# Optimization experiments

Hardware: AMD Instinct MI355X
Metric: run time of the kernel (lower is better)

The kernel has to match this reference:

```python
import jax, jax.numpy as jnp
import numpy as np

N = 100000
E = 800000
NODE_DIM = 128
EDGE_DIM = 8
NUM_HEADS = 8
HEAD_DIM = NODE_DIM // NUM_HEADS


def setup_inputs() -> dict:
    key = jax.random.key(0)
    k_x, k_ei, k_ea, k_w1, k_b1, k_w2, k_b2 = jax.random.split(key, 7)
    x = jax.random.normal(k_x, (N, NODE_DIM), dtype=jnp.float32)
    edge_index = jax.random.randint(k_ei, (2, E), 0, N, dtype=jnp.int32)
    edge_attr = jax.random.normal(k_ea, (E, EDGE_DIM), dtype=jnp.float32)
    # node_proj: Linear(node_dim, node_dim)
    lim1 = 1.0 / np.sqrt(NODE_DIM)
    W_node = jax.random.uniform(k_w1, (NODE_DIM, NODE_DIM), minval=-lim1, maxval=lim1, dtype=jnp.float32)
    b_node = jax.random.uniform(k_b1, (NODE_DIM,), minval=-lim1, maxval=lim1, dtype=jnp.float32)
    # edge_to_attn: Linear(edge_dim, num_heads) followed by sigmoid
    lim2 = 1.0 / np.sqrt(EDGE_DIM)
    W_edge = jax.random.uniform(k_w2, (NUM_HEADS, EDGE_DIM), minval=-lim2, maxval=lim2, dtype=jnp.float32)
    b_edge = jax.random.uniform(k_b2, (NUM_HEADS,), minval=-lim2, maxval=lim2, dtype=jnp.float32)
    return {"x": x, "edge_index": edge_index, "edge_attr": edge_attr,
            "W_node": W_node, "b_node": b_node, "W_edge": W_edge, "b_edge": b_edge}


def reference(x, edge_index, edge_attr, W_node, b_node, W_edge, b_edge):
    # project node features: [N, node_dim]
    x_proj = x @ W_node.T + b_node
    # per-edge, per-head sigmoid gates: [E, H]
    edge_gates = jax.nn.sigmoid(edge_attr @ W_edge.T + b_edge)
    source = edge_index[0]
    target = edge_index[1]
    # gather source node features: [E, H, head_dim]
    x_source = x_proj[source].reshape(E, NUM_HEADS, HEAD_DIM)
    # gate and flatten messages: [E, node_dim]
    messages = (x_source * edge_gates[:, :, None]).reshape(E, NODE_DIM)
    # scatter-add to target nodes: [N, node_dim]
    out = jax.ops.segment_sum(messages, target, num_segments=N)
    return out
```

## Files before the change

### kernel.cpp

```cpp
#include <hip/hip_runtime.h>

typedef unsigned char u8;
typedef unsigned short u16;
typedef unsigned int u32;
typedef __attribute__((ext_vector_type(8))) short short8;
typedef __attribute__((ext_vector_type(4))) float f32x4;

constexpr int NODES = 100000;
constexpr int EDGES = 800000;
constexpr int DIM = 128;
constexpr int EDIM = 8;
constexpr int HEADS = 8;

constexpr int PROJ_BLOCKS = (NODES + 127) / 128;
constexpr int REC_BLOCKS  = (EDGES + 255) / 256;

__device__ inline u16 f2bf(float f) {
    u32 u = __float_as_uint(f);
    u = (u + 0x7FFFu + ((u >> 16) & 1u)) >> 16;
    return (u16)u;
}
__device__ inline float bf2f(u16 s) {
    return __uint_as_float(((u32)s) << 16);
}

__global__ __launch_bounds__(256) void prep_fused(const float* __restrict__ x,
                                                  const float* __restrict__ Wn,
                                                  const float* __restrict__ bn,
                                                  const int* __restrict__ ei,
                                                  const float* __restrict__ ea,
                                                  const float* __restrict__ We,
                                                  const float* __restrict__ be,
                                                  int* __restrict__ head4,
                                                  uint4* __restrict__ recE,
                                                  u16* __restrict__ xpb) {
    __shared__ u16 sLds[64 * 136];

    const int tid = threadIdx.x;

    if (blockIdx.x < PROJ_BLOCKS) {
        if (blockIdx.x == 0 && tid == 0) {
            recE[-1] = uint4{(u32)-1, 0u, 0u, 0u};
        }

        const int w = tid >> 6;
        const int l = tid & 63;
        const int lr = l & 15;
        const int lh = l >> 4;
        const int m0 = blockIdx.x * 128 + w * 32;

        f32x4 acc[2][8];
        #pragma unroll
        for (int mt = 0; mt < 2; ++mt)
            #pragma unroll
            for (int nt = 0; nt < 8; ++nt) acc[mt][nt] = f32x4{0, 0, 0, 0};

        #pragma unroll
        for (int half = 0; half < 2; ++half) {
            __syncthreads();
            {
                #pragma unroll
                for (int i = tid; i < 64 * 16; i += 256) {
                    int row = i >> 4, ch = i & 15;
                    const float* p = Wn + (half * 64 + row) * DIM + ch * 8;
                    float4 f0 = *reinterpret_cast<const float4*>(p);
                    float4 f1 = *reinterpret_cast<const float4*>(p + 4);
                    short8 v;
                    v[0]=(short)f2bf(f0.x); v[1]=(short)f2bf(f0.y);
                    v[2]=(short)f2bf(f0.z); v[3]=(short)f2bf(f0.w);
                    v[4]=(short)f2bf(f1.x); v[5]=(short)f2bf(f1.y);
                    v[6]=(short)f2bf(f1.z); v[7]=(short)f2bf(f1.w);
                    *reinterpret_cast<short8*>(&sLds[row * 136 + ch * 8]) = v;
                }
            }
            __syncthreads();

            #pragma unroll
            for (int kk = 0; kk < 4; ++kk) {
                const int kb = kk * 32 + lh * 8;
                short8 a0, a1;
                {
                    int row = m0 + lr;  row = row < NODES ? row : 0;
                    const float* p = x + (size_t)row * DIM + kb;
                    float4 f0 = *reinterpret_cast<const float4*>(p);
                    float4 f1 = *reinterpret_cast<const float4*>(p + 4);
                    a0[0]=(short)f2bf(f0.x); a0[1]=(short)f2bf(f0.y);
                    a0[2]=(short)f2bf(f0.z); a0[3]=(short)f2bf(f0.w);
                    a0[4]=(short)f2bf(f1.x); a0[5]=(short)f2bf(f1.y);
                    a0[6]=(short)f2bf(f1.z); a0[7]=(short)f2bf(f1.w);
                }
                {
                    int row = m0 + 16 + lr;  row = row < NODES ? row : 0;
                    const float* p = x + (size_t)row * DIM + kb;
                    float4 f0 = *reinterpret_cast<const float4*>(p);
                    float4 f1 = *reinterpret_cast<const float4*>(p + 4);
                    a1[0]=(short)f2bf(f0.x); a1[1]=(short)f2bf(f0.y);
                    a1[2]=(short)f2bf(f0.z); a1[3]=(short)f2bf(f0.w);
                    a1[4]=(short)f2bf(f1.x); a1[5]=(short)f2bf(f1.y);
                    a1[6]=(short)f2bf(f1.z); a1[7]=(short)f2bf(f1.w);
                }
                #pragma unroll
                for (int nt = 0; nt < 4; ++nt) {
                    const int ntg = half * 4 + nt;
                    short8 b = *reinterpret_cast<const short8*>(
                        &sLds[(nt * 16 + lr) * 136 + kb]);
                    acc[0][ntg] = __builtin_amdgcn_mfma_f32_16x16x32_bf16(a0, b, acc[0][ntg], 0, 0, 0);
                    acc[1][ntg] = __builtin_amdgcn_mfma_f32_16x16x32_bf16(a1, b, acc[1][ntg], 0, 0, 0);
                }
            }
        }

        float bias[8];
        #pragma unroll
        for (int nt = 0; nt < 8; ++nt) bias[nt] = bn[nt * 16 + lr];

        #pragma unroll
        for (int mt = 0; mt < 2; ++mt) {
            #pragma unroll
            for (int r = 0; r < 4; ++r) {
                int grow = m0 + mt * 16 + lh * 4 + r;
                if (grow < NODES) {
                    #pragma unroll
                    for (int nt = 0; nt < 8; ++nt)
                        xpb[(size_t)grow * DIM + nt * 16 + lr] =
                            f2bf(acc[mt][nt][r] + bias[nt]);
                }
            }
        }
    } else {
        float* sW = reinterpret_cast<float*>(sLds);
        float* sb = sW + HEADS * EDIM;
        if (tid < HEADS * EDIM) sW[tid] = We[tid];
        if (tid < HEADS) sb[tid] = be[tid];
        __syncthreads();

        const int e = (blockIdx.x - PROJ_BLOCKS) * 256 + tid;
        if (e >= EDGES) return;

        const int src = ei[e];
        const int tgt = ei[EDGES + e];
        float4 a0 = *reinterpret_cast<const float4*>(ea + (size_t)e * EDIM);
        float4 a1 = *reinterpret_cast<const float4*>(ea + (size_t)e * EDIM + 4);

        u32 q[HEADS];
        #pragma unroll
        for (int h = 0; h < HEADS; ++h) {
            const float* w = &sW[h * EDIM];
            float z = sb[h]
                    + a0.x * w[0] + a0.y * w[1] + a0.z * w[2] + a0.w * w[3]
                    + a1.x * w[4] + a1.y * w[5] + a1.z * w[6] + a1.w * w[7];
            float g = 1.0f / (1.0f + __expf(-z));
            q[h] = (u32)(g * 255.0f + 0.5f);
        }

        int nx = atomicExch(&head4[tgt * 4 + (e & 3)], e);

        uint4 r;
        r.x = (u32)nx;
        r.y = (u32)(src * DIM);
        r.z = q[0] | (q[1] << 8) | (q[2] << 16) | (q[3] << 24);
        r.w = q[4] | (q[5] << 8) | (q[6] << 16) | (q[7] << 24);
        recE[e] = r;
    }
}

__global__ __launch_bounds__(256) void aggregate_v10(const u16* __restrict__ xpb,
                                                     const int* __restrict__ head4,
                                                     const uint4* __restrict__ recE,
                                                     float* __restrict__ out) {
    const int n = blockIdx.x * 16 + (threadIdx.x >> 4);
    if (n >= NODES) return;
    const int l = threadIdx.x & 15;
    const int h = l >> 1;
    const int hsh = (h & 3) * 8;
    const bool hlo = (h < 4);

    float acc[8];
    #pragma unroll
    for (int i = 0; i < 8; ++i) acc[i] = 0.0f;

    int e0 = head4[n * 4 + 0];
    int e1 = head4[n * 4 + 1];
    int e2 = head4[n * 4 + 2];
    int e3 = head4[n * 4 + 3];

    while ((e0 & e1 & e2 & e3) != -1) {
        uint4 R0 = recE[(ptrdiff_t)e0];
        uint4 R1 = recE[(ptrdiff_t)e1];
        uint4 R2 = recE[(ptrdiff_t)e2];
        uint4 R3 = recE[(ptrdiff_t)e3];
        float g0 = (float)(((hlo ? R0.z : R0.w) >> hsh) & 0xFF);
        float g1 = (float)(((hlo ? R1.z : R1.w) >> hsh) & 0xFF);
        float g2 = (float)(((hlo ? R2.z : R2.w) >> hsh) & 0xFF);
        float g3 = (float)(((hlo ? R3.z : R3.w) >> hsh) & 0xFF);
        short8 u0 = *reinterpret_cast<const short8*>(xpb + R0.y + l * 8);
        short8 u1 = *reinterpret_cast<const short8*>(xpb + R1.y + l * 8);
        short8 u2 = *reinterpret_cast<const short8*>(xpb + R2.y + l * 8);
        short8 u3 = *reinterpret_cast<const short8*>(xpb + R3.y + l * 8);
        #pragma unroll
        for (int i = 0; i < 8; ++i) {
            acc[i] += g0 * bf2f((u16)u0[i]);
            acc[i] += g1 * bf2f((u16)u1[i]);
            acc[i] += g2 * bf2f((u16)u2[i]);
            acc[i] += g3 * bf2f((u16)u3[i]);
        }
        e0 = (int)R0.x;
        e1 = (int)R1.x;
        e2 = (int)R2.x;
        e3 = (int)R3.x;
    }

    constexpr float DQ = 1.0f / 255.0f;
    float4 o0 = {acc[0] * DQ, acc[1] * DQ, acc[2] * DQ, acc[3] * DQ};
    float4 o1 = {acc[4] * DQ, acc[5] * DQ, acc[6] * DQ, acc[7] * DQ};
    float4* op = reinterpret_cast<float4*>(out + (size_t)n * DIM + l * 8);
    op[0] = o0;
    op[1] = o1;
}

__global__ __launch_bounds__(256) void edge_scatter(const int* __restrict__ ei,
                                                    const float* __restrict__ ea,
                                                    const float* __restrict__ We,
                                                    const float* __restrict__ be,
                                                    const u16* __restrict__ xpb,
                                                    float* __restrict__ out) {
    __shared__ float sW[HEADS * EDIM];
    __shared__ float sb[HEADS];
    if (threadIdx.x < HEADS * EDIM) sW[threadIdx.x] = We[threadIdx.x];
    if (threadIdx.x < HEADS) sb[threadIdx.x] = be[threadIdx.x];
    __syncthreads();

    const int t = blockIdx.x * 256 + threadIdx.x;
    const int e = t >> 5;
    const int l = t & 31;
    if (e >= EDGES) return;

    const int src = ei[e];
    const int tgt = ei[EDGES + e];
    const int h = l >> 2;

    float4 ea0 = *reinterpret_cast<const float4*>(ea + (size_t)e * EDIM);
    float4 ea1 = *reinterpret_cast<const float4*>(ea + (size_t)e * EDIM + 4);
    float4 wa = *reinterpret_cast<const float4*>(&sW[h * EDIM]);
    float4 wb = *reinterpret_cast<const float4*>(&sW[h * EDIM + 4]);
    float z = sb[h]
            + ea0.x * wa.x + ea0.y * wa.y + ea0.z * wa.z + ea0.w * wa.w
            + ea1.x * wb.x + ea1.y * wb.y + ea1.z * wb.z + ea1.w * wb.w;
    float g = 1.0f / (1.0f + __expf(-z));

    ushort4 u = *reinterpret_cast<const ushort4*>(xpb + (size_t)src * DIM + l * 4);
    float* op = out + (size_t)tgt * DIM + l * 4;
    unsafeAtomicAdd(op + 0, bf2f(u.x) * g);
    unsafeAtomicAdd(op + 1, bf2f(u.y) * g);
    unsafeAtomicAdd(op + 2, bf2f(u.z) * g);
    unsafeAtomicAdd(op + 3, bf2f(u.w) * g);
}

extern "C" void kernel_launch(void* const* d_in, const int* in_sizes, int n_in,
                              void* d_out, int out_size, void* d_ws, size_t ws_size,
                              hipStream_t stream) {
    const float* x   = (const float*)d_in[0];
    const int*   ei  = (const int*)d_in[1];
    const float* eat = (const float*)d_in[2];
    const float* Wn  = (const float*)d_in[3];
    const float* bn  = (const float*)d_in[4];
    const float* We  = (const float*)d_in[5];
    const float* be  = (const float*)d_in[6];
    float* out = (float*)d_out;

    u16* xpb   = (u16*)d_ws;
    int* head4 = (int*)(xpb + (size_t)NODES * DIM);
    char* recS = (char*)(head4 + (size_t)NODES * 4);
    uint4* recE = (uint4*)(recS + 16);

    const size_t need = (size_t)NODES * DIM * 2 + (size_t)NODES * 16
                      + (size_t)(EDGES + 1) * 16;
    const size_t need_fb = (size_t)NODES * DIM * 2;

    if (ws_size >= need) {
        hipMemsetAsync(head4, 0xFF, (size_t)NODES * 16, stream);
        prep_fused<<<PROJ_BLOCKS + REC_BLOCKS, 256, 0, stream>>>(
            x, Wn, bn, ei, eat, We, be, head4, recE, xpb);
        aggregate_v10<<<(NODES + 15) / 16, 256, 0, stream>>>(xpb, head4, recE, out);
    } else if (ws_size >= need_fb) {
        prep_fused<<<PROJ_BLOCKS, 256, 0, stream>>>(
            x, Wn, bn, ei, eat, We, be, nullptr, recE, xpb);
        hipMemsetAsync(d_out, 0, (size_t)out_size * sizeof(float), stream);
        edge_scatter<<<(EDGES * 32) / 256, 256, 0, stream>>>(ei, eat, We, be, xpb, out);
    }
}
```

Before: 112.7 us.

## Split fused prep kernel, fold head init into projection, stage stores via LDS

Splits the fused projection/edge-record kernel into a dedicated MFMA projection kernel and a separate edge-record kernel. The projection kernel now initializes the head4 list heads itself, replacing the memset launch, and loads the whole bf16 weight matrix into LDS once instead of in two halves. Output tiles are staged through LDS so each row is written with 16-byte global stores rather than scattered 2-byte ones. In exchange it adds a kernel boundary where projection and edge work could previously overlap, and uses more LDS per block, which may lower occupancy.

```diff
diff --git a/kernel.cpp b/kernel.cpp
--- a/kernel.cpp
+++ b/kernel.cpp
@@ -12,9 +12,6 @@
 constexpr int EDIM = 8;
 constexpr int HEADS = 8;
 
-constexpr int PROJ_BLOCKS = (NODES + 127) / 128;
-constexpr int REC_BLOCKS  = (EDGES + 255) / 256;
-
 __device__ inline u16 f2bf(float f) {
     u32 u = __float_as_uint(f);
     u = (u + 0x7FFFu + ((u >> 16) & 1u)) >> 16;
@@ -24,144 +21,154 @@
     return __uint_as_float(((u32)s) << 16);
 }
 
-__global__ __launch_bounds__(256) void prep_fused(const float* __restrict__ x,
-                                                  const float* __restrict__ Wn,
-                                                  const float* __restrict__ bn,
-                                                  const int* __restrict__ ei,
-                                                  const float* __restrict__ ea,
-                                                  const float* __restrict__ We,
-                                                  const float* __restrict__ be,
-                                                  int* __restrict__ head4,
-                                                  uint4* __restrict__ recE,
-                                                  u16* __restrict__ xpb) {
-    __shared__ u16 sLds[64 * 136];
+__global__ __launch_bounds__(256) void node_proj_mfma(const float* __restrict__ x,
+                                                      const float* __restrict__ Wn,
+                                                      const float* __restrict__ bn,
+                                                      u16* __restrict__ xpb,
+                                                      int* __restrict__ head4,
+                                                      uint4* __restrict__ recE) {
+    __shared__ u16 sW[128 * 136];
 
     const int tid = threadIdx.x;
 
-    if (blockIdx.x < PROJ_BLOCKS) {
-        if (blockIdx.x == 0 && tid == 0) {
+    if (head4 != nullptr) {
+        int t = blockIdx.x * 256 + tid;
+        if (t < NODES * 2) {
+            head4[2 * t] = -1;
+            head4[2 * t + 1] = -1;
+        }
+        if (blockIdx.x == 0 && tid == 0)
             recE[-1] = uint4{(u32)-1, 0u, 0u, 0u};
-        }
-
-        const int w = tid >> 6;
-        const int l = tid & 63;
-        const int lr = l & 15;
-        const int lh = l >> 4;
-        const int m0 = blockIdx.x * 128 + w * 32;
-
-        f32x4 acc[2][8];
-        #pragma unroll
-        for (int mt = 0; mt < 2; ++mt)
+    }
+
+    {
+        #pragma unroll
+        for (int i = tid; i < 128 * 16; i += 256) {
+            int row = i >> 4, ch = i & 15;
+            const float* p = Wn + row * DIM + ch * 8;
+            float4 f0 = *reinterpret_cast<const float4*>(p);
+            float4 f1 = *reinterpret_cast<const float4*>(p + 4);
+            short8 v;
+            v[0]=(short)f2bf(f0.x); v[1]=(short)f2bf(f0.y);
+            v[2]=(short)f2bf(f0.z); v[3]=(short)f2bf(f0.w);
+            v[4]=(short)f2bf(f1.x); v[5]=(short)f2bf(f1.y);
+            v[6]=(short)f2bf(f1.z); v[7]=(short)f2bf(f1.w);
+            *reinterpret_cast<short8*>(&sW[row * 136 + ch * 8]) = v;
+        }
+    }
+    __syncthreads();
+
+    const int w = tid >> 6;
+    const int l = tid & 63;
+    const int lr = l & 15;
+    const int lh = l >> 4;
+    const int m0 = blockIdx.x * 128 + w * 32;
+
+    f32x4 acc[2][8];
+    #pragma unroll
+    for (int mt = 0; mt < 2; ++mt)
+        #pragma unroll
+        for (int nt = 0; nt < 8; ++nt) acc[mt][nt] = f32x4{0, 0, 0, 0};
+
+    #pragma unroll
+    for (int kk = 0; kk < 4; ++kk) {
+        const int kb = kk * 32 + lh * 8;
+        short8 a0, a1;
+        {
+            int row = m0 + lr;  row = row < NODES ? row : 0;
+            const float* p = x + (size_t)row * DIM + kb;
+            float4 f0 = *reinterpret_cast<const float4*>(p);
+            float4 f1 = *reinterpret_cast<const float4*>(p + 4);
+            a0[0]=(short)f2bf(f0.x); a0[1]=(short)f2bf(f0.y);
+            a0[2]=(short)f2bf(f0.z); a0[3]=(short)f2bf(f0.w);
+            a0[4]=(short)f2bf(f1.x); a0[5]=(short)f2bf(f1.y);
+            a0[6]=(short)f2bf(f1.z); a0[7]=(short)f2bf(f1.w);
+        }
+        {
+            int row = m0 + 16 + lr;  row = row < NODES ? row : 0;
+            const float* p = x + (size_t)row * DIM + kb;
+            float4 f0 = *reinterpret_cast<const float4*>(p);
+            float4 f1 = *reinterpret_cast<const float4*>(p + 4);
+            a1[0]=(short)f2bf(f0.x); a1[1]=(short)f2bf(f0.y);
+            a1[2]=(short)f2bf(f0.z); a1[3]=(short)f2bf(f0.w);
+            a1[4]=(short)f2bf(f1.x); a1[5]=(short)f2bf(f1.y);
+            a1[6]=(short)f2bf(f1.z); a1[7]=(short)f2bf(f1.w);
+        }
+        #pragma unroll
+        for (int nt = 0; nt < 8; ++nt) {
+            short8 b = *reinterpret_cast<const short8*>(&sW[(nt * 16 + lr) * 136 + kb]);
+            acc[0][nt] = __builtin_amdgcn_mfma_f32_16x16x32_bf16(a0, b, acc[0][nt], 0, 0, 0);
+            acc[1][nt] = __builtin_amdgcn_mfma_f32_16x16x32_bf16(a1, b, acc[1][nt], 0, 0, 0);
+        }
+    }
+
+    float bias[8];
+    #pragma unroll
+    for (int nt = 0; nt < 8; ++nt) bias[nt] = bn[nt * 16 + lr];
+
+    __syncthreads();
+    u16* sT = sW + w * (32 * 136);
+
+    #pragma unroll
+    for (int mt = 0; mt < 2; ++mt)
+        #pragma unroll
+        for (int r = 0; r < 4; ++r)
             #pragma unroll
-            for (int nt = 0; nt < 8; ++nt) acc[mt][nt] = f32x4{0, 0, 0, 0};
-
-        #pragma unroll
-        for (int half = 0; half < 2; ++half) {
-            __syncthreads();
-            {
-                #pragma unroll
-                for (int i = tid; i < 64 * 16; i += 256) {
-                    int row = i >> 4, ch = i & 15;
-                    const float* p = Wn + (half * 64 + row) * DIM + ch * 8;
-                    float4 f0 = *reinterpret_cast<const float4*>(p);
-                    float4 f1 = *reinterpret_cast<const float4*>(p + 4);
-                    short8 v;
-                    v[0]=(short)f2bf(f0.x); v[1]=(short)f2bf(f0.y);
-                    v[2]=(short)f2bf(f0.z); v[3]=(short)f2bf(f0.w);
-                    v[4]=(short)f2bf(f1.x); v[5]=(short)f2bf(f1.y);
-                    v[6]=(short)f2bf(f1.z); v[7]=(short)f2bf(f1.w);
-                    *reinterpret_cast<short8*>(&sLds[row * 136 + ch * 8]) = v;
-                }
-            }
-            __syncthreads();
-
-            #pragma unroll
-            for (int kk = 0; kk < 4; ++kk) {
-                const int kb = kk * 32 + lh * 8;
-                short8 a0, a1;
-                {
-                    int row = m0 + lr;  row = row < NODES ? row : 0;
-                    const float* p = x + (size_t)row * DIM + kb;
-                    float4 f0 = *reinterpret_cast<const float4*>(p);
-                    float4 f1 = *reinterpret_cast<const float4*>(p + 4);
-                    a0[0]=(short)f2bf(f0.x); a0[1]=(short)f2bf(f0.y);
-                    a0[2]=(short)f2bf(f0.z); a0[3]=(short)f2bf(f0.w);
-                    a0[4]=(short)f2bf(f1.x); a0[5]=(short)f2bf(f1.y);
-                    a0[6]=(short)f2bf(f1.z); a0[7]=(short)f2bf(f1.w);
-                }
-                {
-                    int row = m0 + 16 + lr;  row = row < NODES ? row : 0;
-                    const float* p = x + (size_t)row * DIM + kb;
-                    float4 f0 = *reinterpret_cast<const float4*>(p);
-                    float4 f1 = *reinterpret_cast<const float4*>(p + 4);
-                    a1[0]=(short)f2bf(f0.x); a1[1]=(short)f2bf(f0.y);
-                    a1[2]=(short)f2bf(f0.z); a1[3]=(short)f2bf(f0.w);
-                    a1[4]=(short)f2bf(f1.x); a1[5]=(short)f2bf(f1.y);
-                    a1[6]=(short)f2bf(f1.z); a1[7]=(short)f2bf(f1.w);
-                }
-                #pragma unroll
-                for (int nt = 0; nt < 4; ++nt) {
-                    const int ntg = half * 4 + nt;
-                    short8 b = *reinterpret_cast<const short8*>(
-                        &sLds[(nt * 16 + lr) * 136 + kb]);
-                    acc[0][ntg] = __builtin_amdgcn_mfma_f32_16x16x32_bf16(a0, b, acc[0][ntg], 0, 0, 0);
-                    acc[1][ntg] = __builtin_amdgcn_mfma_f32_16x16x32_bf16(a1, b, acc[1][ntg], 0, 0, 0);
-                }
-            }
-        }
-
-        float bias[8];
-        #pragma unroll
-        for (int nt = 0; nt < 8; ++nt) bias[nt] = bn[nt * 16 + lr];
-
-        #pragma unroll
-        for (int mt = 0; mt < 2; ++mt) {
-            #pragma unroll
-            for (int r = 0; r < 4; ++r) {
-                int grow = m0 + mt * 16 + lh * 4 + r;
-                if (grow < NODES) {
-                    #pragma unroll
-                    for (int nt = 0; nt < 8; ++nt)
-                        xpb[(size_t)grow * DIM + nt * 16 + lr] =
-                            f2bf(acc[mt][nt][r] + bias[nt]);
-                }
-            }
-        }
-    } else {
-        float* sW = reinterpret_cast<float*>(sLds);
-        float* sb = sW + HEADS * EDIM;
-        if (tid < HEADS * EDIM) sW[tid] = We[tid];
-        if (tid < HEADS) sb[tid] = be[tid];
-        __syncthreads();
-
-        const int e = (blockIdx.x - PROJ_BLOCKS) * 256 + tid;
-        if (e >= EDGES) return;
-
-        const int src = ei[e];
-        const int tgt = ei[EDGES + e];
-        float4 a0 = *reinterpret_cast<const float4*>(ea + (size_t)e * EDIM);
-        float4 a1 = *reinterpret_cast<const float4*>(ea + (size_t)e * EDIM + 4);
-
-        u32 q[HEADS];
-        #pragma unroll
-        for (int h = 0; h < HEADS; ++h) {
-            const float* w = &sW[h * EDIM];
-            float z = sb[h]
-                    + a0.x * w[0] + a0.y * w[1] + a0.z * w[2] + a0.w * w[3]
-                    + a1.x * w[4] + a1.y * w[5] + a1.z * w[6] + a1.w * w[7];
-            float g = 1.0f / (1.0f + __expf(-z));
-            q[h] = (u32)(g * 255.0f + 0.5f);
-        }
-
-        int nx = atomicExch(&head4[tgt * 4 + (e & 3)], e);
-
-        uint4 r;
-        r.x = (u32)nx;
-        r.y = (u32)(src * DIM);
-        r.z = q[0] | (q[1] << 8) | (q[2] << 16) | (q[3] << 24);
-        r.w = q[4] | (q[5] << 8) | (q[6] << 16) | (q[7] << 24);
-        recE[e] = r;
-    }
+            for (int nt = 0; nt < 8; ++nt)
+                sT[(mt * 16 + lh * 4 + r) * 136 + nt * 16 + lr] =
+                    f2bf(acc[mt][nt][r] + bias[nt]);
+
+    #pragma unroll
+    for (int i = 0; i < 8; ++i) {
+        int flat = i * 64 + l;
+        int row = flat >> 4;
+        int ch  = flat & 15;
+        short8 v = *reinterpret_cast<const short8*>(&sT[row * 136 + ch * 8]);
+        int grow = m0 + row;
+        if (grow < NODES)
+            *reinterpret_cast<short8*>(&xpb[(size_t)grow * DIM + ch * 8]) = v;
+    }
+}
+
+__global__ __launch_bounds__(256) void build_rec(const int* __restrict__ ei,
+                                                 const float* __restrict__ ea,
+                                                 const float* __restrict__ We,
+                                                 const float* __restrict__ be,
+                                                 int* __restrict__ head4,
+                                                 uint4* __restrict__ recE) {
+    __shared__ float sW[HEADS * EDIM];
+    __shared__ float sb[HEADS];
+    if (threadIdx.x < HEADS * EDIM) sW[threadIdx.x] = We[threadIdx.x];
+    if (threadIdx.x < HEADS) sb[threadIdx.x] = be[threadIdx.x];
+    __syncthreads();
+
+    const int e = blockIdx.x * 256 + threadIdx.x;
+    if (e >= EDGES) return;
+
+    const int src = ei[e];
+    const int tgt = ei[EDGES + e];
+    float4 a0 = *reinterpret_cast<const float4*>(ea + (size_t)e * EDIM);
+    float4 a1 = *reinterpret_cast<const float4*>(ea + (size_t)e * EDIM + 4);
+
+    u32 q[HEADS];
+    #pragma unroll
+    for (int h = 0; h < HEADS; ++h) {
+        const float* w = &sW[h * EDIM];
+        float z = sb[h]
+                + a0.x * w[0] + a0.y * w[1] + a0.z * w[2] + a0.w * w[3]
+                + a1.x * w[4] + a1.y * w[5] + a1.z * w[6] + a1.w * w[7];
+        float g = 1.0f / (1.0f + __expf(-z));
+        q[h] = (u32)(g * 255.0f + 0.5f);
+    }
+
+    int nx = atomicExch(&head4[tgt * 4 + (e & 3)], e);
+
+    uint4 r;
+    r.x = (u32)nx;
+    r.y = (u32)(src * DIM);
+    r.z = q[0] | (q[1] << 8) | (q[2] << 16) | (q[3] << 24);
+    r.w = q[4] | (q[5] << 8) | (q[6] << 16) | (q[7] << 24);
+    recE[e] = r;
 }
 
 __global__ __launch_bounds__(256) void aggregate_v10(const u16* __restrict__ xpb,
@@ -278,13 +285,14 @@
     const size_t need_fb = (size_t)NODES * DIM * 2;
 
     if (ws_size >= need) {
-        hipMemsetAsync(head4, 0xFF, (size_t)NODES * 16, stream);
-        prep_fused<<<PROJ_BLOCKS + REC_BLOCKS, 256, 0, stream>>>(
-            x, Wn, bn, ei, eat, We, be, head4, recE, xpb);
+        node_proj_mfma<<<(NODES + 127) / 128, 256, 0, stream>>>(x, Wn, bn, xpb,
+                                                                head4, recE);
+        build_rec<<<(EDGES + 255) / 256, 256, 0, stream>>>(ei, eat, We, be,
+                                                           head4, recE);
         aggregate_v10<<<(NODES + 15) / 16, 256, 0, stream>>>(xpb, head4, recE, out);
     } else if (ws_size >= need_fb) {
-        prep_fused<<<PROJ_BLOCKS, 256, 0, stream>>>(
-            x, Wn, bn, ei, eat, We, be, nullptr, recE, xpb);
+        node_proj_mfma<<<(NODES + 127) / 128, 256, 0, stream>>>(x, Wn, bn, xpb,
+                                                                nullptr, nullptr);
         hipMemsetAsync(d_out, 0, (size_t)out_size * sizeof(float), stream);
         edge_scatter<<<(EDGES * 32) / 256, 256, 0, stream>>>(ei, eat, We, be, xpb, out);
     }
```

Result: no change. 112.1 us (-0.6%).
